# Optimization experiments

Measured on AMD Instinct MI355X. Metric: run time of the kernel, lower is better.

Reference implementation:

```python
import jax, jax.numpy as jnp
import numpy as np

B, T, I, H, L, O = 256, 256, 512, 1024, 2, 1


def setup_inputs() -> dict:
    key = jax.random.key(0)
    ks = jax.random.split(key, 8)
    s_i = 1.0 / np.sqrt(I)
    s_h = 1.0 / np.sqrt(H)
    return {
        "init_hidden": jax.random.normal(ks[0], (B, H), jnp.float32),
        "context": jax.random.normal(ks[1], (B, T, I), jnp.float32),
        "W_ih0": jax.random.normal(ks[2], (4 * H, I), jnp.float32) * s_i,
        "W_hh0": jax.random.normal(ks[3], (4 * H, H), jnp.float32) * s_h,
        "b_ih0": jnp.zeros((4 * H,), jnp.float32),
        "b_hh0": jnp.zeros((4 * H,), jnp.float32),
        "W_ih1": jax.random.normal(ks[4], (4 * H, H), jnp.float32) * s_h,
        "W_hh1": jax.random.normal(ks[5], (4 * H, H), jnp.float32) * s_h,
        "b_ih1": jnp.zeros((4 * H,), jnp.float32),
        "b_hh1": jnp.zeros((4 * H,), jnp.float32),
        "W_ro": jax.random.normal(ks[6], (O, H), jnp.float32) * s_h,
        "b_ro": jnp.zeros((O,), jnp.float32),
    }


def _lstm_layer(x, h0, c0, W_ih, W_hh, b_ih, b_hh):
    """x: [B,T,Din] -> all hidden states [B,T,H]. PyTorch gate order i,f,g,o."""
    # Precompute input contribution for all timesteps (one big GEMM).
    xg = jnp.einsum('btd,gd->btg', x, W_ih) + b_ih + b_hh  # [B,T,4H]

    def step(carry, xg_t):
        h, c = carry
        gates = xg_t + h @ W_hh.T                          # [B,4H]
        i, f, g, o = jnp.split(gates, 4, axis=-1)
        i = jax.nn.sigmoid(i)
        f = jax.nn.sigmoid(f)
        g = jnp.tanh(g)
        o = jax.nn.sigmoid(o)
        c = f * c + i * g
        h = o * jnp.tanh(c)
        return (h, c), h

    (_, _), hs = jax.lax.scan(step, (h0, c0), jnp.swapaxes(xg, 0, 1))
    return jnp.swapaxes(hs, 0, 1)  # [B,T,H]


def reference(init_hidden, context, W_ih0, W_hh0, b_ih0, b_hh0,
              W_ih1, W_hh1, b_ih1, b_hh1, W_ro, b_ro):
    c0 = jnp.zeros((context.shape[0], H), context.dtype)
    # h0 for every layer is the same init_hidden (torch.stack of init_hidden).
    h1 = _lstm_layer(context, init_hidden, c0, W_ih0, W_hh0, b_ih0, b_hh0)
    h2 = _lstm_layer(h1, init_hidden, c0, W_ih1, W_hh1, b_ih1, b_hh1)
    # readout on last timestep -> [B, O]
    return h2[:, -1, :] @ W_ro.T + b_ro
```

## Files before the change

kernel.cpp:

```cpp
#include <hip/hip_runtime.h>
#include <hip/hip_bf16.h>

#define B_ 256
#define T_ 256
#define I_ 512
#define H_ 1024
#define CH 8
#define NCH 32

typedef _Float16 half8 __attribute__((ext_vector_type(8)));
typedef float floatx4 __attribute__((ext_vector_type(4)));

__device__ __forceinline__ float fsig(float x) {
  return 1.f / (1.f + __expf(-x));
}
__device__ __forceinline__ float ftanh(float x) {
  return 1.f - 2.f / (__expf(2.f * x) + 1.f);
}


__global__ __launch_bounds__(256) void prep_w(
    _Float16* __restrict__ dst, const float* __restrict__ src, int K) {
  const int np = blockIdx.y;
  const int k = blockIdx.x * 256 + threadIdx.x;
  const int cc = np & 63, g = cc >> 4, j = cc & 15;
  const int orig = g * H_ + (np >> 6) * 16 + j;
  dst[(size_t)np * K + k] = (_Float16)src[(size_t)orig * K + k];
}

__global__ __launch_bounds__(256) void prep_bias(
    float* __restrict__ bs0, float* __restrict__ bs1,
    const float* __restrict__ bih0, const float* __restrict__ bhh0,
    const float* __restrict__ bih1, const float* __restrict__ bhh1) {
  const int np = blockIdx.x * 256 + threadIdx.x;
  const int cc = np & 63, g = cc >> 4, j = cc & 15;
  const int orig = g * H_ + (np >> 6) * 16 + j;
  bs0[np] = bih0[orig] + bhh0[orig];
  bs1[np] = bih1[orig] + bhh1[orig];
}

__global__ __launch_bounds__(256) void prep_state(
    const float* __restrict__ init, _Float16* __restrict__ h1s,
    _Float16* __restrict__ h2s, float* __restrict__ c0, float* __restrict__ c1) {
  const int idx = blockIdx.x * 256 + threadIdx.x;
  const float v = init[idx];
  h1s[B_ * H_ + idx] = (_Float16)v;
  h2s[B_ * H_ + idx] = (_Float16)v;
  c0[idx] = 0.f;
  c1[idx] = 0.f;
}

template<int KK, int AMODE>
__global__ __launch_bounds__(256, 2) void gemm_xg(
    const void* __restrict__ Ap, const _Float16* __restrict__ Bw,
    const float* __restrict__ bias, _Float16* __restrict__ out, int tbase) {
  constexpr int NST = KK / 64;
  __shared__ _Float16 As[2][128 * 72];
  __shared__ _Float16 Bs[2][128 * 72];
  const int tid = threadIdx.x;
  const int row0 = blockIdx.x * 128, col0 = blockIdx.y * 128;
  const int sr = tid >> 1, sc = (tid & 1) * 32;
  const int gr = row0 + sr;
  const size_t arow = (AMODE == 0)
      ? ((size_t)(gr & 255) * T_ + (size_t)tbase + (gr >> 8)) * I_
      : (size_t)gr * KK;
  const float*    af32 = (const float*)Ap + arow + sc;
  const _Float16* af16 = (const _Float16*)Ap + arow + sc;
  const _Float16* bsrc = Bw + (size_t)(col0 + sr) * KK + sc;

  const int w = tid >> 6, lane = tid & 63;
  const int wm = (w >> 1) * 64, wn = (w & 1) * 64;
  const int l15 = lane & 15, kg = (lane >> 4) * 8;
  floatx4 acc[4][4] = {};
  half8 ar[4], br[4];

  auto load_stage = [&](int ki) {
    const int k = ki * 64;
    #pragma unroll
    for (int c = 0; c < 4; ++c) {
      if (AMODE == 0) {
        float4 f0 = *(const float4*)(af32 + k + c * 8);
        float4 f1 = *(const float4*)(af32 + k + c * 8 + 4);
        half8 h;
        h[0] = (_Float16)f0.x; h[1] = (_Float16)f0.y;
        h[2] = (_Float16)f0.z; h[3] = (_Float16)f0.w;
        h[4] = (_Float16)f1.x; h[5] = (_Float16)f1.y;
        h[6] = (_Float16)f1.z; h[7] = (_Float16)f1.w;
        ar[c] = h;
      } else {
        ar[c] = *(const half8*)(af16 + k + c * 8);
      }
      br[c] = *(const half8*)(bsrc + k + c * 8);
    }
  };
  auto write_stage = [&](int buf) {
    #pragma unroll
    for (int c = 0; c < 4; ++c) *(half8*)(&As[buf][sr * 72 + sc + c * 8]) = ar[c];
    #pragma unroll
    for (int c = 0; c < 4; ++c) *(half8*)(&Bs[buf][sr * 72 + sc + c * 8]) = br[c];
  };

  load_stage(0); write_stage(0); __syncthreads();
  for (int ki = 0; ki < NST; ++ki) {
    const int cur = ki & 1;
    if (ki + 1 < NST) load_stage(ki + 1);
    #pragma unroll
    for (int ks = 0; ks < 2; ++ks) {
      half8 bf[4];
      #pragma unroll
      for (int n = 0; n < 4; ++n)
        bf[n] = *(const half8*)(&Bs[cur][(wn + 16 * n + l15) * 72 + ks * 32 + kg]);
      #pragma unroll
      for (int m = 0; m < 4; ++m) {
        half8 af = *(const half8*)(&As[cur][(wm + 16 * m + l15) * 72 + ks * 32 + kg]);
        #pragma unroll
        for (int n = 0; n < 4; ++n)
          acc[m][n] = __builtin_amdgcn_mfma_f32_16x16x32_f16(af, bf[n], acc[m][n], 0, 0, 0);
      }
    }
    if (ki + 1 < NST) write_stage(cur ^ 1);
    __syncthreads();
  }

  const int crow = (lane >> 4) * 4;
  #pragma unroll
  for (int n = 0; n < 4; ++n) {
    const int col = col0 + wn + 16 * n + l15;
    const float bv = bias[col];
    #pragma unroll
    for (int m = 0; m < 4; ++m) {
      const int rbase = row0 + wm + 16 * m + crow;
      #pragma unroll
      for (int r = 0; r < 4; ++r)
        out[(size_t)(rbase + r) * 4096 + col] = (_Float16)(acc[m][n][r] + bv);
    }
  }
}

__global__ __launch_bounds__(256) void lstm_step(
    const _Float16* __restrict__ Wh0, const _Float16* __restrict__ Wh1,
    const _Float16* __restrict__ xg0, const _Float16* __restrict__ xg1,
    _Float16* __restrict__ h1s, _Float16* __restrict__ h2s,
    _Float16* __restrict__ h1chunk, float* __restrict__ c0buf,
    float* __restrict__ c1buf, float* __restrict__ hF, int t0, int t1, int ci) {
  const int bid = blockIdx.x;
  const int layer = bid >> 7;
  const int t = layer ? t1 : t0;
  if (t < 0) return;
  const int b7 = bid & 127;
  const int row0 = (b7 >> 6) * 128;
  const int nb = b7 & 63;
  const int col0 = nb * 64;
  const _Float16* __restrict__ Wh = layer ? Wh1 : Wh0;
  const _Float16* __restrict__ xg = (layer ? xg1 : xg0) + (size_t)ci * 256 * 4096;
  _Float16* __restrict__ hs = layer ? h2s : h1s;
  float* __restrict__ cbuf = layer ? c1buf : c0buf;
  const int rd = (t + 1) & 1, wr = t & 1;
  const _Float16* __restrict__ hin = hs + rd * (B_ * H_);

  __shared__ _Float16 As[2][128 * 72];
  __shared__ _Float16 Bs[2][64 * 72];

  const int tid = threadIdx.x;
  const int srow = tid >> 3;
  const int spc = (tid & 7) * 8;
  const _Float16* asrc = hin + (size_t)(row0 + srow) * H_ + spc;
  const _Float16* bsrc = Wh + (size_t)(col0 + srow) * H_ + spc;
  half8 ar[4], br[2];

  auto load_stage = [&](int ki) {
    const int k = ki * 64;
    #pragma unroll
    for (int p = 0; p < 4; ++p) ar[p] = *(const half8*)(asrc + (size_t)(p * 32) * H_ + k);
    #pragma unroll
    for (int p = 0; p < 2; ++p) br[p] = *(const half8*)(bsrc + (size_t)(p * 32) * H_ + k);
  };
  auto write_stage = [&](int buf) {
    #pragma unroll
    for (int p = 0; p < 4; ++p) *(half8*)(&As[buf][(srow + p * 32) * 72 + spc]) = ar[p];
    #pragma unroll
    for (int p = 0; p < 2; ++p) *(half8*)(&Bs[buf][(srow + p * 32) * 72 + spc]) = br[p];
  };

  const int w = tid >> 6, lane = tid & 63;
  const int l15 = lane & 15, kg = (lane >> 4) * 8;
  const int wrow = w * 32;
  floatx4 acc[2][4] = {};

  load_stage(0); write_stage(0); __syncthreads();
  for (int ki = 0; ki < 16; ++ki) {
    const int cur = ki & 1;
    if (ki < 15) load_stage(ki + 1);
    #pragma unroll
    for (int ks = 0; ks < 2; ++ks) {
      half8 bf[4];
      #pragma unroll
      for (int n = 0; n < 4; ++n)
        bf[n] = *(const half8*)(&Bs[cur][(16 * n + l15) * 72 + ks * 32 + kg]);
      #pragma unroll
      for (int m = 0; m < 2; ++m) {
        half8 af = *(const half8*)(&As[cur][(wrow + 16 * m + l15) * 72 + ks * 32 + kg]);
        #pragma unroll
        for (int n = 0; n < 4; ++n)
          acc[m][n] = __builtin_amdgcn_mfma_f32_16x16x32_f16(af, bf[n], acc[m][n], 0, 0, 0);
      }
    }
    if (ki < 15) write_stage(cur ^ 1);
    __syncthreads();
  }

  const int hu = nb * 16 + l15;
  const int rsub = (lane >> 4) * 4;
  #pragma unroll
  for (int m = 0; m < 2; ++m) {
    #pragma unroll
    for (int r = 0; r < 4; ++r) {
      const int brow = row0 + wrow + 16 * m + rsub + r;
      const _Float16* xr = xg + (size_t)brow * 4096 + col0;
      const float gi = acc[m][0][r] + (float)xr[l15];
      const float gf = acc[m][1][r] + (float)xr[16 + l15];
      const float gg = acc[m][2][r] + (float)xr[32 + l15];
      const float go = acc[m][3][r] + (float)xr[48 + l15];
      const float si = fsig(gi);
      const float sf = fsig(gf);
      const float so = fsig(go);
      const float tg = ftanh(gg);
      const size_t cidx = (size_t)brow * H_ + hu;
      const float cn = sf * cbuf[cidx] + si * tg;
      const float hn = so * ftanh(cn);
      cbuf[cidx] = cn;
      hs[wr * (B_ * H_) + cidx] = (_Float16)hn;
      if (layer == 0)
        h1chunk[((size_t)ci * 256 + brow) * H_ + hu] = (_Float16)hn;
      else
        hF[cidx] = hn;
    }
  }
}

__global__ __launch_bounds__(256) void readout(
    const float* __restrict__ hF, const float* __restrict__ Wro,
    const float* __restrict__ bro, float* __restrict__ out) {
  const int b = blockIdx.x;
  const int tid = threadIdx.x;
  float p = 0.f;
  for (int h = tid; h < H_; h += 256) p += hF[(size_t)b * H_ + h] * Wro[h];
  #pragma unroll
  for (int off = 32; off; off >>= 1) p += __shfl_down(p, off, 64);
  __shared__ float red[4];
  if ((tid & 63) == 0) red[tid >> 6] = p;
  __syncthreads();
  if (tid == 0) out[b] = red[0] + red[1] + red[2] + red[3] + bro[0];
}

extern "C" void kernel_launch(void* const* d_in, const int* in_sizes, int n_in,
                              void* d_out, int out_size, void* d_ws, size_t ws_size,
                              hipStream_t stream) {
  const float* init_hidden = (const float*)d_in[0];
  const float* ctx   = (const float*)d_in[1];
  const float* W_ih0 = (const float*)d_in[2];
  const float* W_hh0 = (const float*)d_in[3];
  const float* b_ih0 = (const float*)d_in[4];
  const float* b_hh0 = (const float*)d_in[5];
  const float* W_ih1 = (const float*)d_in[6];
  const float* W_hh1 = (const float*)d_in[7];
  const float* b_ih1 = (const float*)d_in[8];
  const float* b_hh1 = (const float*)d_in[9];
  const float* W_ro  = (const float*)d_in[10];
  const float* b_ro  = (const float*)d_in[11];

  char* ws = (char*)d_ws;
  _Float16* W0p  = (_Float16*)(ws);
  _Float16* Wh0p = (_Float16*)(ws + 4194304);
  _Float16* W1p  = (_Float16*)(ws + 12582912);
  _Float16* Wh1p = (_Float16*)(ws + 20971520);
  float*    bs0  = (float*)(ws + 29360128);
  float*    bs1  = (float*)(ws + 29376512);
  _Float16* xg0  = (_Float16*)(ws + 29392896);
  _Float16* xg1  = (_Float16*)(ws + 46170112);
  _Float16* h1c  = (_Float16*)(ws + 62947328);
  _Float16* h1s  = (_Float16*)(ws + 67141632);
  _Float16* h2s  = (_Float16*)(ws + 68190208);
  float*    c0   = (float*)(ws + 69238784);
  float*    c1   = (float*)(ws + 70287360);
  float*    hF   = (float*)(ws + 71335936);

  prep_w<<<dim3(I_ / 256, 4096), 256, 0, stream>>>(W0p, W_ih0, I_);
  prep_w<<<dim3(H_ / 256, 4096), 256, 0, stream>>>(Wh0p, W_hh0, H_);
  prep_w<<<dim3(H_ / 256, 4096), 256, 0, stream>>>(W1p, W_ih1, H_);
  prep_w<<<dim3(H_ / 256, 4096), 256, 0, stream>>>(Wh1p, W_hh1, H_);
  prep_bias<<<dim3(16), 256, 0, stream>>>(bs0, bs1, b_ih0, b_hh0, b_ih1, b_hh1);
  prep_state<<<dim3(B_ * H_ / 256), 256, 0, stream>>>(init_hidden, h1s, h2s, c0, c1);

  for (int c = 0; c <= NCH; ++c) {
    if (c < NCH)
      gemm_xg<512, 0><<<dim3(16, 32), 256, 0, stream>>>(ctx, W0p, bs0, xg0, c * CH);
    if (c >= 1)
      gemm_xg<1024, 1><<<dim3(16, 32), 256, 0, stream>>>(h1c, W1p, bs1, xg1, 0);
    for (int i = 0; i < CH; ++i) {
      const int t0 = (c < NCH) ? c * CH + i : -1;
      const int t1 = (c >= 1) ? (c - 1) * CH + i : -1;
      lstm_step<<<dim3(256), 256, 0, stream>>>(Wh0p, Wh1p, xg0, xg1, h1s, h2s,
                                               h1c, c0, c1, hF, t0, t1, i);
    }
  }
  readout<<<dim3(B_), 256, 0, stream>>>(hF, W_ro, b_ro, (float*)d_out);
}
```

Before: 6.533 ms.

## Replace per-step kernel launches with persistent megakernel using grid barriers

Collapses the chunked input-GEMM launches and the per-timestep LSTM kernels into a single persistent kernel of 256 blocks that loops over wavefront steps, separated by a software grid barrier. Each block keeps its slice of the recurrent weights resident in shared memory (128 KB of fp16) and holds its input-projection weights and cell state in registers. The input projections for the next step are computed by the same blocks, with double-buffered xg and h rings. The aim is to remove launch overhead and repeated weight reloads from global memory. In exchange it relies on all 256 blocks being co-resident, adds spin-barrier latency at every step, and puts heavy pressure on registers and LDS.

```diff
diff --git a/kernel.cpp b/kernel.cpp
--- a/kernel.cpp
+++ b/kernel.cpp
@@ -5,18 +5,13 @@
 #define T_ 256
 #define I_ 512
 #define H_ 1024
-#define CH 8
-#define NCH 32
 
 typedef _Float16 half8 __attribute__((ext_vector_type(8)));
+typedef _Float16 half4 __attribute__((ext_vector_type(4)));
 typedef float floatx4 __attribute__((ext_vector_type(4)));
 
-__device__ __forceinline__ float fsig(float x) {
-  return 1.f / (1.f + __expf(-x));
-}
-__device__ __forceinline__ float ftanh(float x) {
-  return 1.f - 2.f / (__expf(2.f * x) + 1.f);
-}
+__device__ __forceinline__ float fsig(float x) { return 1.f / (1.f + __expf(-x)); }
+__device__ __forceinline__ float ftanh(float x) { return 1.f - 2.f / (__expf(2.f * x) + 1.f); }
 
 
 __global__ __launch_bounds__(256) void prep_w(
@@ -39,201 +34,224 @@
   bs1[np] = bih1[orig] + bhh1[orig];
 }
 
-__global__ __launch_bounds__(256) void prep_state(
-    const float* __restrict__ init, _Float16* __restrict__ h1s,
-    _Float16* __restrict__ h2s, float* __restrict__ c0, float* __restrict__ c1) {
-  const int idx = blockIdx.x * 256 + threadIdx.x;
-  const float v = init[idx];
-  h1s[B_ * H_ + idx] = (_Float16)v;
-  h2s[B_ * H_ + idx] = (_Float16)v;
-  c0[idx] = 0.f;
-  c1[idx] = 0.f;
-}
-
-template<int KK, int AMODE>
-__global__ __launch_bounds__(256, 2) void gemm_xg(
-    const void* __restrict__ Ap, const _Float16* __restrict__ Bw,
-    const float* __restrict__ bias, _Float16* __restrict__ out, int tbase) {
-  constexpr int NST = KK / 64;
-  __shared__ _Float16 As[2][128 * 72];
-  __shared__ _Float16 Bs[2][128 * 72];
+struct MegaArgs {
+  const float* ctx;
+  const _Float16* W0p;  const _Float16* W1p;
+  const _Float16* Wh0p; const _Float16* Wh1p;
+  const float* bs0; const float* bs1;
+  _Float16* h1ring; _Float16* h2ring;
+  _Float16* xg0ring; _Float16* xg1ring;
+  float* hF;
+  const float* init;
+  unsigned* bar;
+};
+
+__device__ __forceinline__ void gridbar(unsigned* bar) {
+  __syncthreads();
+  if (threadIdx.x == 0) {
+    unsigned* cnt = bar;
+    unsigned* gen = bar + 16;
+    unsigned g = __hip_atomic_load(gen, __ATOMIC_RELAXED, __HIP_MEMORY_SCOPE_AGENT);
+    unsigned a = __hip_atomic_fetch_add(cnt, 1u, __ATOMIC_ACQ_REL, __HIP_MEMORY_SCOPE_AGENT);
+    if (a == 255u) {
+      __hip_atomic_store(cnt, 0u, __ATOMIC_RELAXED, __HIP_MEMORY_SCOPE_AGENT);
+      __hip_atomic_store(gen, g + 1u, __ATOMIC_RELEASE, __HIP_MEMORY_SCOPE_AGENT);
+    } else {
+      while (__hip_atomic_load(gen, __ATOMIC_ACQUIRE, __HIP_MEMORY_SCOPE_AGENT) == g)
+        __builtin_amdgcn_s_sleep(1);
+    }
+  }
+  __syncthreads();
+}
+
+template<int NC, int AMODE>
+__device__ __forceinline__ void gemm_tile(
+    const void* __restrict__ aptr, const half8* __restrict__ bf,
+    _Float16* __restrict__ ab, floatx4 (&gacc)[8]) {
   const int tid = threadIdx.x;
-  const int row0 = blockIdx.x * 128, col0 = blockIdx.y * 128;
-  const int sr = tid >> 1, sc = (tid & 1) * 32;
-  const int gr = row0 + sr;
-  const size_t arow = (AMODE == 0)
-      ? ((size_t)(gr & 255) * T_ + (size_t)tbase + (gr >> 8)) * I_
-      : (size_t)gr * KK;
-  const float*    af32 = (const float*)Ap + arow + sc;
-  const _Float16* af16 = (const _Float16*)Ap + arow + sc;
-  const _Float16* bsrc = Bw + (size_t)(col0 + sr) * KK + sc;
-
-  const int w = tid >> 6, lane = tid & 63;
-  const int wm = (w >> 1) * 64, wn = (w & 1) * 64;
-  const int l15 = lane & 15, kg = (lane >> 4) * 8;
-  floatx4 acc[4][4] = {};
-  half8 ar[4], br[4];
-
-  auto load_stage = [&](int ki) {
-    const int k = ki * 64;
-    #pragma unroll
-    for (int c = 0; c < 4; ++c) {
+  const int srow = tid >> 1;
+  const int lane = tid & 63, l15 = lane & 15, l4 = lane >> 4;
+  const float*    af32 = (const float*)aptr;
+  const _Float16* af16 = (const _Float16*)aptr;
+  half8 st[2][4];
+  auto fetch = [&](int c, int slot) {
+    #pragma unroll
+    for (int p = 0; p < 4; ++p) {
       if (AMODE == 0) {
-        float4 f0 = *(const float4*)(af32 + k + c * 8);
-        float4 f1 = *(const float4*)(af32 + k + c * 8 + 4);
+        float4 f0 = *(const float4*)(af32 + c * 64 + p * 8);
+        float4 f1 = *(const float4*)(af32 + c * 64 + p * 8 + 4);
         half8 h;
         h[0] = (_Float16)f0.x; h[1] = (_Float16)f0.y;
         h[2] = (_Float16)f0.z; h[3] = (_Float16)f0.w;
         h[4] = (_Float16)f1.x; h[5] = (_Float16)f1.y;
         h[6] = (_Float16)f1.z; h[7] = (_Float16)f1.w;
-        ar[c] = h;
+        st[slot][p] = h;
       } else {
-        ar[c] = *(const half8*)(af16 + k + c * 8);
-      }
-      br[c] = *(const half8*)(bsrc + k + c * 8);
+        st[slot][p] = *(const half8*)(af16 + c * 64 + p * 8);
+      }
     }
   };
-  auto write_stage = [&](int buf) {
-    #pragma unroll
-    for (int c = 0; c < 4; ++c) *(half8*)(&As[buf][sr * 72 + sc + c * 8]) = ar[c];
-    #pragma unroll
-    for (int c = 0; c < 4; ++c) *(half8*)(&Bs[buf][sr * 72 + sc + c * 8]) = br[c];
-  };
-
-  load_stage(0); write_stage(0); __syncthreads();
-  for (int ki = 0; ki < NST; ++ki) {
-    const int cur = ki & 1;
-    if (ki + 1 < NST) load_stage(ki + 1);
-    #pragma unroll
-    for (int ks = 0; ks < 2; ++ks) {
-      half8 bf[4];
-      #pragma unroll
-      for (int n = 0; n < 4; ++n)
-        bf[n] = *(const half8*)(&Bs[cur][(wn + 16 * n + l15) * 72 + ks * 32 + kg]);
-      #pragma unroll
-      for (int m = 0; m < 4; ++m) {
-        half8 af = *(const half8*)(&As[cur][(wm + 16 * m + l15) * 72 + ks * 32 + kg]);
+  fetch(0, 0);
+  fetch(1, 1);
+  #pragma unroll
+  for (int c = 0; c < NC; ++c) {
+    __syncthreads();
+    #pragma unroll
+    for (int p = 0; p < 4; ++p) {
+      const int g = (tid & 1) * 4 + p;
+      *(half8*)(ab + srow * 64 + ((g ^ (srow & 7)) * 8)) = st[c & 1][p];
+    }
+    __syncthreads();
+    if (c + 2 < NC) fetch(c + 2, c & 1);
+    #pragma unroll
+    for (int ks2 = 0; ks2 < 2; ++ks2) {
+      #pragma unroll
+      for (int m = 0; m < 8; ++m) {
+        const int arow = m * 16 + l15;
+        const int ga = ks2 * 4 + l4;
+        half8 af = *(const half8*)(ab + arow * 64 + ((ga ^ (arow & 7)) * 8));
+        gacc[m] = __builtin_amdgcn_mfma_f32_16x16x32_f16(af, bf[c * 2 + ks2], gacc[m], 0, 0, 0);
+      }
+    }
+  }
+}
+
+__global__ __launch_bounds__(256, 1) void mega(MegaArgs a) {
+  const int bid = blockIdx.x, tid = threadIdx.x;
+  const int layer = bid >> 7, strip = (bid >> 6) & 1, nb = bid & 63;
+  const int row0 = strip * 128;
+  const int w = tid >> 6, lane = tid & 63, l15 = lane & 15, l4 = lane >> 4;
+
+  __shared__ _Float16 whb[64 * 1024];
+  __shared__ _Float16 ab[128 * 64];
+
+  {
+    const int idx = (bid * 256 + tid) * 4;
+    const float4 v = *(const float4*)(a.init + idx);
+    half4 hv; hv[0] = (_Float16)v.x; hv[1] = (_Float16)v.y;
+    hv[2] = (_Float16)v.z; hv[3] = (_Float16)v.w;
+    *(half4*)(a.h1ring + B_ * H_ + idx) = hv;
+    *(half4*)(a.h2ring + B_ * H_ + idx) = hv;
+  }
+
+  {
+    const _Float16* Whp = (layer ? a.Wh1p : a.Wh0p) + (size_t)nb * 64 * 1024;
+    const int row = tid & 63;
+    const int gb = (tid >> 6) * 32;
+    #pragma unroll
+    for (int i = 0; i < 32; ++i) {
+      const int g = gb + i;
+      half8 v = *(const half8*)(Whp + (size_t)row * 1024 + g * 8);
+      *(half8*)(whb + row * 1024 + ((g ^ (row & 7)) * 8)) = v;
+    }
+  }
+
+  const _Float16* Wg = layer ? a.W1p : a.W0p;
+  const int gK = layer ? 1024 : 512;
+  const int gcol = nb * 64 + w * 16 + l15;
+  half8 bf[32];
+  {
+    const int nks = layer ? 32 : 16;
+    #pragma unroll
+    for (int ks = 0; ks < 32; ++ks)
+      if (ks < nks)
+        bf[ks] = *(const half8*)(Wg + (size_t)gcol * gK + ks * 32 + l4 * 8);
+  }
+  const float bv = (layer ? a.bs1 : a.bs0)[gcol];
+
+  float cst[8] = {0.f, 0.f, 0.f, 0.f, 0.f, 0.f, 0.f, 0.f};
+  const int hu = nb * 16 + l15;
+  const int srow = tid >> 1;
+  const int scol = (tid & 1) * 32;
+
+  for (int s = 0; s <= 258; ++s) {
+    gridbar(a.bar);
+    const bool recAct = layer ? (s >= 3 && s <= 258) : (s >= 1 && s <= 256);
+    if (recAct) {
+      const _Float16* Asrc = (layer ? a.h2ring : a.h1ring) + (size_t)(s & 1) * (B_ * H_);
+      const _Float16* xg = (layer ? a.xg1ring : a.xg0ring) + (size_t)((s - 1) & 1) * (B_ * 4096);
+      const _Float16* abase = Asrc + (size_t)(row0 + srow) * H_ + scol;
+      floatx4 racc[2][4] = {};
+      half8 st[2][4];
+      #pragma unroll
+      for (int p = 0; p < 4; ++p) st[0][p] = *(const half8*)(abase + 0 * 64 + p * 8);
+      #pragma unroll
+      for (int p = 0; p < 4; ++p) st[1][p] = *(const half8*)(abase + 1 * 64 + p * 8);
+      #pragma unroll
+      for (int c = 0; c < 16; ++c) {
+        __syncthreads();
         #pragma unroll
-        for (int n = 0; n < 4; ++n)
-          acc[m][n] = __builtin_amdgcn_mfma_f32_16x16x32_f16(af, bf[n], acc[m][n], 0, 0, 0);
-      }
-    }
-    if (ki + 1 < NST) write_stage(cur ^ 1);
+        for (int p = 0; p < 4; ++p) {
+          const int g = (tid & 1) * 4 + p;
+          *(half8*)(ab + srow * 64 + ((g ^ (srow & 7)) * 8)) = st[c & 1][p];
+        }
+        __syncthreads();
+        if (c + 2 < 16) {
+          #pragma unroll
+          for (int p = 0; p < 4; ++p)
+            st[c & 1][p] = *(const half8*)(abase + (c + 2) * 64 + p * 8);
+        }
+        #pragma unroll
+        for (int ks2 = 0; ks2 < 2; ++ks2) {
+          half8 wbf[4];
+          #pragma unroll
+          for (int n = 0; n < 4; ++n) {
+            const int wrow = n * 16 + l15;
+            const int g = c * 8 + ks2 * 4 + l4;
+            wbf[n] = *(const half8*)(whb + wrow * 1024 + ((g ^ (wrow & 7)) * 8));
+          }
+          #pragma unroll
+          for (int m = 0; m < 2; ++m) {
+            const int arow = w * 32 + m * 16 + l15;
+            const int ga = ks2 * 4 + l4;
+            half8 af = *(const half8*)(ab + arow * 64 + ((ga ^ (arow & 7)) * 8));
+            #pragma unroll
+            for (int n = 0; n < 4; ++n)
+              racc[m][n] = __builtin_amdgcn_mfma_f32_16x16x32_f16(af, wbf[n], racc[m][n], 0, 0, 0);
+          }
+        }
+      }
+      const int t = layer ? (s - 3) : (s - 1);
+      _Float16* hw = (layer ? a.h2ring : a.h1ring) + (size_t)((s - 1) & 1) * (B_ * H_);
+      #pragma unroll
+      for (int m = 0; m < 2; ++m) {
+        #pragma unroll
+        for (int r = 0; r < 4; ++r) {
+          const int brow = row0 + w * 32 + m * 16 + l4 * 4 + r;
+          const _Float16* xr = xg + (size_t)brow * 4096 + nb * 64;
+          const float gi = racc[m][0][r] + (float)xr[l15];
+          const float gf = racc[m][1][r] + (float)xr[16 + l15];
+          const float gg = racc[m][2][r] + (float)xr[32 + l15];
+          const float go = racc[m][3][r] + (float)xr[48 + l15];
+          const float si = fsig(gi), sf = fsig(gf), so = fsig(go);
+          const float tg = ftanh(gg);
+          const float cn = sf * cst[m * 4 + r] + si * tg;
+          const float hn = so * ftanh(cn);
+          cst[m * 4 + r] = cn;
+          hw[(size_t)brow * H_ + hu] = (_Float16)hn;
+          if (layer == 1 && t == 255) a.hF[(size_t)brow * H_ + hu] = hn;
+        }
+      }
+    }
     __syncthreads();
-  }
-
-  const int crow = (lane >> 4) * 4;
-  #pragma unroll
-  for (int n = 0; n < 4; ++n) {
-    const int col = col0 + wn + 16 * n + l15;
-    const float bv = bias[col];
-    #pragma unroll
-    for (int m = 0; m < 4; ++m) {
-      const int rbase = row0 + wm + 16 * m + crow;
-      #pragma unroll
-      for (int r = 0; r < 4; ++r)
-        out[(size_t)(rbase + r) * 4096 + col] = (_Float16)(acc[m][n][r] + bv);
-    }
-  }
-}
-
-__global__ __launch_bounds__(256) void lstm_step(
-    const _Float16* __restrict__ Wh0, const _Float16* __restrict__ Wh1,
-    const _Float16* __restrict__ xg0, const _Float16* __restrict__ xg1,
-    _Float16* __restrict__ h1s, _Float16* __restrict__ h2s,
-    _Float16* __restrict__ h1chunk, float* __restrict__ c0buf,
-    float* __restrict__ c1buf, float* __restrict__ hF, int t0, int t1, int ci) {
-  const int bid = blockIdx.x;
-  const int layer = bid >> 7;
-  const int t = layer ? t1 : t0;
-  if (t < 0) return;
-  const int b7 = bid & 127;
-  const int row0 = (b7 >> 6) * 128;
-  const int nb = b7 & 63;
-  const int col0 = nb * 64;
-  const _Float16* __restrict__ Wh = layer ? Wh1 : Wh0;
-  const _Float16* __restrict__ xg = (layer ? xg1 : xg0) + (size_t)ci * 256 * 4096;
-  _Float16* __restrict__ hs = layer ? h2s : h1s;
-  float* __restrict__ cbuf = layer ? c1buf : c0buf;
-  const int rd = (t + 1) & 1, wr = t & 1;
-  const _Float16* __restrict__ hin = hs + rd * (B_ * H_);
-
-  __shared__ _Float16 As[2][128 * 72];
-  __shared__ _Float16 Bs[2][64 * 72];
-
-  const int tid = threadIdx.x;
-  const int srow = tid >> 3;
-  const int spc = (tid & 7) * 8;
-  const _Float16* asrc = hin + (size_t)(row0 + srow) * H_ + spc;
-  const _Float16* bsrc = Wh + (size_t)(col0 + srow) * H_ + spc;
-  half8 ar[4], br[2];
-
-  auto load_stage = [&](int ki) {
-    const int k = ki * 64;
-    #pragma unroll
-    for (int p = 0; p < 4; ++p) ar[p] = *(const half8*)(asrc + (size_t)(p * 32) * H_ + k);
-    #pragma unroll
-    for (int p = 0; p < 2; ++p) br[p] = *(const half8*)(bsrc + (size_t)(p * 32) * H_ + k);
-  };
-  auto write_stage = [&](int buf) {
-    #pragma unroll
-    for (int p = 0; p < 4; ++p) *(half8*)(&As[buf][(srow + p * 32) * 72 + spc]) = ar[p];
-    #pragma unroll
-    for (int p = 0; p < 2; ++p) *(half8*)(&Bs[buf][(srow + p * 32) * 72 + spc]) = br[p];
-  };
-
-  const int w = tid >> 6, lane = tid & 63;
-  const int l15 = lane & 15, kg = (lane >> 4) * 8;
-  const int wrow = w * 32;
-  floatx4 acc[2][4] = {};
-
-  load_stage(0); write_stage(0); __syncthreads();
-  for (int ki = 0; ki < 16; ++ki) {
-    const int cur = ki & 1;
-    if (ki < 15) load_stage(ki + 1);
-    #pragma unroll
-    for (int ks = 0; ks < 2; ++ks) {
-      half8 bf[4];
-      #pragma unroll
-      for (int n = 0; n < 4; ++n)
-        bf[n] = *(const half8*)(&Bs[cur][(16 * n + l15) * 72 + ks * 32 + kg]);
-      #pragma unroll
-      for (int m = 0; m < 2; ++m) {
-        half8 af = *(const half8*)(&As[cur][(wrow + 16 * m + l15) * 72 + ks * 32 + kg]);
+    const bool gAct = layer ? (s >= 2 && s <= 257) : (s <= 255);
+    if (gAct) {
+      _Float16* og = (layer ? a.xg1ring : a.xg0ring) + (size_t)(s & 1) * (B_ * 4096);
+      floatx4 gacc[8] = {};
+      if (layer) {
+        const _Float16* abase = a.h1ring + (size_t)(s & 1) * (B_ * H_)
+                              + (size_t)(row0 + srow) * H_ + scol;
+        gemm_tile<16, 1>(abase, bf, ab, gacc);
+      } else {
+        const float* abase = a.ctx + ((size_t)(row0 + srow) * T_ + s) * I_ + scol;
+        gemm_tile<8, 0>(abase, bf, ab, gacc);
+      }
+      #pragma unroll
+      for (int m = 0; m < 8; ++m) {
         #pragma unroll
-        for (int n = 0; n < 4; ++n)
-          acc[m][n] = __builtin_amdgcn_mfma_f32_16x16x32_f16(af, bf[n], acc[m][n], 0, 0, 0);
-      }
-    }
-    if (ki < 15) write_stage(cur ^ 1);
-    __syncthreads();
-  }
-
-  const int hu = nb * 16 + l15;
-  const int rsub = (lane >> 4) * 4;
-  #pragma unroll
-  for (int m = 0; m < 2; ++m) {
-    #pragma unroll
-    for (int r = 0; r < 4; ++r) {
-      const int brow = row0 + wrow + 16 * m + rsub + r;
-      const _Float16* xr = xg + (size_t)brow * 4096 + col0;
-      const float gi = acc[m][0][r] + (float)xr[l15];
-      const float gf = acc[m][1][r] + (float)xr[16 + l15];
-      const float gg = acc[m][2][r] + (float)xr[32 + l15];
-      const float go = acc[m][3][r] + (float)xr[48 + l15];
-      const float si = fsig(gi);
-      const float sf = fsig(gf);
-      const float so = fsig(go);
-      const float tg = ftanh(gg);
-      const size_t cidx = (size_t)brow * H_ + hu;
-      const float cn = sf * cbuf[cidx] + si * tg;
-      const float hn = so * ftanh(cn);
-      cbuf[cidx] = cn;
-      hs[wr * (B_ * H_) + cidx] = (_Float16)hn;
-      if (layer == 0)
-        h1chunk[((size_t)ci * 256 + brow) * H_ + hu] = (_Float16)hn;
-      else
-        hF[cidx] = hn;
+        for (int r = 0; r < 4; ++r)
+          og[(size_t)(row0 + m * 16 + l4 * 4 + r) * 4096 + gcol] = (_Float16)(gacc[m][r] + bv);
+      }
     }
   }
 }
@@ -270,39 +288,33 @@
   const float* b_ro  = (const float*)d_in[11];
 
   char* ws = (char*)d_ws;
-  _Float16* W0p  = (_Float16*)(ws);
-  _Float16* Wh0p = (_Float16*)(ws + 4194304);
-  _Float16* W1p  = (_Float16*)(ws + 12582912);
-  _Float16* Wh1p = (_Float16*)(ws + 20971520);
-  float*    bs0  = (float*)(ws + 29360128);
-  float*    bs1  = (float*)(ws + 29376512);
-  _Float16* xg0  = (_Float16*)(ws + 29392896);
-  _Float16* xg1  = (_Float16*)(ws + 46170112);
-  _Float16* h1c  = (_Float16*)(ws + 62947328);
-  _Float16* h1s  = (_Float16*)(ws + 67141632);
-  _Float16* h2s  = (_Float16*)(ws + 68190208);
-  float*    c0   = (float*)(ws + 69238784);
-  float*    c1   = (float*)(ws + 70287360);
-  float*    hF   = (float*)(ws + 71335936);
-
-  prep_w<<<dim3(I_ / 256, 4096), 256, 0, stream>>>(W0p, W_ih0, I_);
-  prep_w<<<dim3(H_ / 256, 4096), 256, 0, stream>>>(Wh0p, W_hh0, H_);
-  prep_w<<<dim3(H_ / 256, 4096), 256, 0, stream>>>(W1p, W_ih1, H_);
-  prep_w<<<dim3(H_ / 256, 4096), 256, 0, stream>>>(Wh1p, W_hh1, H_);
+  const size_t MB = 1 << 20;
+  _Float16* W0p    = (_Float16*)(ws);
+  _Float16* Wh0p   = (_Float16*)(ws + 4 * MB);
+  _Float16* W1p    = (_Float16*)(ws + 12 * MB);
+  _Float16* Wh1p   = (_Float16*)(ws + 20 * MB);
+  float*    bs0    = (float*)(ws + 28 * MB);
+  float*    bs1    = (float*)(ws + 28 * MB + 16384);
+  float*    hF     = (float*)(ws + 28 * MB + 32768);
+  _Float16* h1ring = (_Float16*)(ws + 29 * MB + 32768);
+  _Float16* h2ring = (_Float16*)(ws + 30 * MB + 32768);
+  _Float16* xg0    = (_Float16*)(ws + 31 * MB + 32768);
+  _Float16* xg1    = (_Float16*)(ws + 35 * MB + 32768);
+  unsigned* bar    = (unsigned*)(ws + 39 * MB + 32768);
+
+  hipMemsetAsync(bar, 0, 128, stream);
+  prep_w<<<dim3(2, 4096), 256, 0, stream>>>(W0p, W_ih0, 512);
+  prep_w<<<dim3(4, 4096), 256, 0, stream>>>(Wh0p, W_hh0, 1024);
+  prep_w<<<dim3(4, 4096), 256, 0, stream>>>(W1p, W_ih1, 1024);
+  prep_w<<<dim3(4, 4096), 256, 0, stream>>>(Wh1p, W_hh1, 1024);
   prep_bias<<<dim3(16), 256, 0, stream>>>(bs0, bs1, b_ih0, b_hh0, b_ih1, b_hh1);
-  prep_state<<<dim3(B_ * H_ / 256), 256, 0, stream>>>(init_hidden, h1s, h2s, c0, c1);
-
-  for (int c = 0; c <= NCH; ++c) {
-    if (c < NCH)
-      gemm_xg<512, 0><<<dim3(16, 32), 256, 0, stream>>>(ctx, W0p, bs0, xg0, c * CH);
-    if (c >= 1)
-      gemm_xg<1024, 1><<<dim3(16, 32), 256, 0, stream>>>(h1c, W1p, bs1, xg1, 0);
-    for (int i = 0; i < CH; ++i) {
-      const int t0 = (c < NCH) ? c * CH + i : -1;
-      const int t1 = (c >= 1) ? (c - 1) * CH + i : -1;
-      lstm_step<<<dim3(256), 256, 0, stream>>>(Wh0p, Wh1p, xg0, xg1, h1s, h2s,
-                                               h1c, c0, c1, hF, t0, t1, i);
-    }
-  }
-  readout<<<dim3(B_), 256, 0, stream>>>(hF, W_ro, b_ro, (float*)d_out);
-}
+
+  MegaArgs ma;
+  ma.ctx = ctx; ma.W0p = W0p; ma.W1p = W1p; ma.Wh0p = Wh0p; ma.Wh1p = Wh1p;
+  ma.bs0 = bs0; ma.bs1 = bs1; ma.h1ring = h1ring; ma.h2ring = h2ring;
+  ma.xg0ring = xg0; ma.xg1ring = xg1; ma.hF = hF; ma.init = init_hidden;
+  ma.bar = bar;
+  mega<<<dim3(256), dim3(256), 0, stream>>>(ma);
+
+  readout<<<dim3(256), 256, 0, stream>>>(hF, W_ro, b_ro, (float*)d_out);
+}
```

Result: slower. 15.70 ms (+140.3%).
